# Optimization experiments

Measured on AMD Instinct MI355X. Metric: run time of the kernel, lower is better.

Reference implementation:

```python
import jax, jax.numpy as jnp
import numpy as np

N_NODES = 100000


def _gcn_layer(x, W, b, src, dst, num_nodes):
    """GCNConv: out = D^-1/2 (A+I) D^-1/2 (x @ W) + b.
    src/dst already include self-loops."""
    h = x @ W  # [N, out]
    ones = jnp.ones(src.shape[0], dtype=x.dtype)
    deg = jax.ops.segment_sum(ones, dst, num_segments=num_nodes)  # in-degree incl. self-loop
    dinv = jnp.where(deg > 0, jax.lax.rsqrt(deg), 0.0)
    norm = dinv[src] * dinv[dst]  # [E]
    msg = h[src] * norm[:, None]  # gather + scale, [E, out]
    out = jax.ops.segment_sum(msg, dst, num_segments=num_nodes)  # scatter-add
    return out + b


def setup_inputs() -> dict:
    key = jax.random.key(0)
    k1, k2, k3, k4, k5, k6 = jax.random.split(key, 6)
    in_c, hid_c, out_c = 128, 128, 64  # hidden = 2*out_channels
    n_edges = 1600000
    x = jax.random.normal(k1, (N_NODES, in_c), dtype=jnp.float32)
    edge_index = jax.random.randint(k2, (2, n_edges), 0, N_NODES, dtype=jnp.int64)
    s = 1.0 / np.sqrt(in_c)
    W1 = jax.random.uniform(k3, (in_c, hid_c), jnp.float32, -s, s)
    b1 = jnp.zeros((hid_c,), jnp.float32)
    s2 = 1.0 / np.sqrt(hid_c)
    W2 = jax.random.uniform(k4, (hid_c, out_c), jnp.float32, -s2, s2)
    b2 = jnp.zeros((out_c,), jnp.float32)
    return {"x": x, "edge_index": edge_index, "W1": W1, "b1": b1, "W2": W2, "b2": b2}


def reference(x, edge_index, W1, b1, W2, b2):
    num_nodes = x.shape[0]
    loops = jnp.arange(num_nodes, dtype=edge_index.dtype)
    src = jnp.concatenate([edge_index[0], loops])
    dst = jnp.concatenate([edge_index[1], loops])
    h = jax.nn.relu(_gcn_layer(x, W1, b1, src, dst, num_nodes))
    return _gcn_layer(h, W2, b2, src, dst, num_nodes)
```

## Files before the change

### kernel.cpp

```cpp
#include <hip/hip_runtime.h>
#include <hip/hip_bf16.h>


typedef short bf16x8 __attribute__((ext_vector_type(8)));
typedef float f32x4 __attribute__((ext_vector_type(4)));

__device__ __forceinline__ unsigned pack_bf16_2(float a, float b) {
    unsigned ua = __builtin_bit_cast(unsigned, a);
    unsigned ub = __builtin_bit_cast(unsigned, b);
    ua += 0x7FFFu + ((ua >> 16) & 1u);
    ub += 0x7FFFu + ((ub >> 16) & 1u);
    return (ua >> 16) | (ub & 0xFFFF0000u);
}
__device__ __forceinline__ unsigned short bf16_1(float a) {
    unsigned ua = __builtin_bit_cast(unsigned, a);
    ua += 0x7FFFu + ((ua >> 16) & 1u);
    return (unsigned short)(ua >> 16);
}
__device__ __forceinline__ float bf16_lo(unsigned v) {
    return __builtin_bit_cast(float, v << 16);
}
__device__ __forceinline__ float bf16_hi(unsigned v) {
    return __builtin_bit_cast(float, v & 0xFFFF0000u);
}

__global__ __launch_bounds__(256) void partition_fixed(const int* __restrict__ src,
                                                       const int* __restrict__ dst,
                                                       int* __restrict__ bcur,
                                                       int2* __restrict__ ebuf,
                                                       int E, int nb, int cap) {
    __shared__ int hist[256];
    __shared__ int basel[256];
    const int tid = threadIdx.x;
    const int c0 = blockIdx.x * 4096;
    for (int t = tid; t < nb; t += 256) hist[t] = 0;
    __syncthreads();
    int s[16], d[16], r[16];
#pragma unroll
    for (int i = 0; i < 16; ++i) {
        int idx = c0 + i * 256 + tid;
        if (idx < E) {
            s[i] = src[idx];
            d[i] = dst[idx];
            r[i] = atomicAdd(&hist[d[i] >> 10], 1);
        } else {
            d[i] = -1;
        }
    }
    __syncthreads();
    for (int t = tid; t < nb; t += 256) basel[t] = hist[t] ? atomicAdd(&bcur[t], hist[t]) : 0;
    __syncthreads();
#pragma unroll
    for (int i = 0; i < 16; ++i) {
        if (d[i] >= 0) {
            int b = d[i] >> 10;
            int pos = basel[b] + r[i];
            if (pos < cap)
                ebuf[(size_t)b * cap + pos] = make_int2(s[i], d[i]);
        }
    }
}

__global__ __launch_bounds__(256) void csr_build(const int2* __restrict__ ebuf,
                                                 const int* __restrict__ bcur,
                                                 int* __restrict__ offs,
                                                 float* __restrict__ dinv,
                                                 int* __restrict__ csr,
                                                 int N, int E, int nb, int cap) {
    __shared__ int hist[1024];
    __shared__ int lofs[1024];
    __shared__ int stmp[256];
    __shared__ int s_e0, s_cnt;
    const int b = blockIdx.x;
    const int tid = threadIdx.x;
    const int n0 = b << 10;

    {
        int bc = (tid < nb) ? bcur[tid] : 0;
        stmp[tid] = bc;
        __syncthreads();
        int run = bc;
        for (int off = 1; off < 256; off <<= 1) {
            int t = (tid >= off) ? stmp[tid - off] : 0;
            __syncthreads();
            run += t;
            stmp[tid] = run;
            __syncthreads();
        }
        if (tid == b) { s_cnt = bc; s_e0 = run - bc; }
        __syncthreads();
    }
    const int e0 = s_e0;
    const int cnt = s_cnt;
    const int2* eb = ebuf + (size_t)b * cap;

#pragma unroll
    for (int q = 0; q < 4; ++q) hist[tid + q * 256] = 0;
    __syncthreads();
    for (int e = tid; e < cnt; e += 256)
        atomicAdd(&hist[eb[e].y & 1023], 1);
    __syncthreads();
    const int base4 = tid * 4;
    int v[4];
#pragma unroll
    for (int q = 0; q < 4; ++q) v[q] = hist[base4 + q];
    const int tsum = v[0] + v[1] + v[2] + v[3];
    stmp[tid] = tsum;
    __syncthreads();
    int run = tsum;
    for (int off = 1; off < 256; off <<= 1) {
        int t = (tid >= off) ? stmp[tid - off] : 0;
        __syncthreads();
        run += t;
        stmp[tid] = run;
        __syncthreads();
    }
    int s = run - tsum;
#pragma unroll
    for (int q = 0; q < 4; ++q) { lofs[base4 + q] = s; s += v[q]; }
    __syncthreads();
#pragma unroll
    for (int q = 0; q < 4; ++q) {
        int il = tid + q * 256;
        int node = n0 + il;
        if (node < N) {
            offs[node] = e0 + lofs[il];
            dinv[node] = rsqrtf((float)(hist[il] + 1));
        }
    }
    __syncthreads();
    for (int e = tid; e < cnt; e += 256) {
        int2 p = eb[e];
        int pos = atomicAdd(&lofs[p.y & 1023], 1);
        csr[e0 + pos] = p.x;
    }
    if (b == 0 && tid == 0) offs[N] = E;
}

template <int COUT, bool INBF16>
__global__ __launch_bounds__(256) void gemm_mfma(const void* __restrict__ Xv,
                                                 const float* __restrict__ W,
                                                 const float* __restrict__ dinv,
                                                 unsigned short* __restrict__ Gs, int N) {
    constexpr int BR = 64;
    constexpr int CPT = COUT / 16;
    __shared__ unsigned short sx[BR][136];
    __shared__ unsigned short swT[COUT][136];
    const int tid = threadIdx.x;
    const int r0 = blockIdx.x * BR;

    if constexpr (INBF16) {
        const unsigned* Xb = (const unsigned*)Xv;
#pragma unroll
        for (int q = 0; q < 4; ++q) {
            int off = q * 1024 + tid * 4;
            int row = off >> 6;
            int ku = off & 63;
            size_t grow = (size_t)min(r0 + row, N - 1);
            uint4 v = *reinterpret_cast<const uint4*>(&Xb[grow * 64 + ku]);
            *reinterpret_cast<uint4*>(&sx[row][ku * 2]) = v;
        }
    } else {
        const float* Xf = (const float*)Xv;
#pragma unroll
        for (int q = 0; q < 8; ++q) {
            int off = q * 1024 + tid * 4;
            int row = off >> 7;
            int k = off & 127;
            size_t grow = (size_t)min(r0 + row, N - 1);
            float4 v = *reinterpret_cast<const float4*>(&Xf[grow * 128 + k]);
            uint2 pk;
            pk.x = pack_bf16_2(v.x, v.y);
            pk.y = pack_bf16_2(v.z, v.w);
            *reinterpret_cast<uint2*>(&sx[row][k]) = pk;
        }
    }
#pragma unroll
    for (int q = 0; q < COUT / 8; ++q) {
        int off = q * 1024 + tid * 4;
        int k = off / COUT;
        int c = off % COUT;
        float4 v = *reinterpret_cast<const float4*>(&W[off]);
        swT[c + 0][k] = bf16_1(v.x);
        swT[c + 1][k] = bf16_1(v.y);
        swT[c + 2][k] = bf16_1(v.z);
        swT[c + 3][k] = bf16_1(v.w);
    }
    __syncthreads();

    const int w = tid >> 6;
    const int l = tid & 63;
    const int lr = l & 15;
    const int lkg = l >> 4;
    f32x4 acc[CPT];
#pragma unroll
    for (int c = 0; c < CPT; ++c) acc[c] = f32x4{0.f, 0.f, 0.f, 0.f};

#pragma unroll
    for (int ks = 0; ks < 4; ++ks) {
        const int k0 = ks * 32 + lkg * 8;
        bf16x8 a = *reinterpret_cast<const bf16x8*>(&sx[w * 16 + lr][k0]);
#pragma unroll
        for (int c = 0; c < CPT; ++c) {
            bf16x8 b = *reinterpret_cast<const bf16x8*>(&swT[c * 16 + lr][k0]);
            acc[c] = __builtin_amdgcn_mfma_f32_16x16x32_bf16(a, b, acc[c], 0, 0, 0);
        }
    }

#pragma unroll
    for (int r = 0; r < 4; ++r) {
        int gr = r0 + w * 16 + lkg * 4 + r;
        if (gr < N) {
            float di = dinv[gr];
#pragma unroll
            for (int c = 0; c < CPT; ++c)
                Gs[(size_t)gr * COUT + c * 16 + lr] = bf16_1(acc[c][r] * di);
        }
    }
}

__global__ __launch_bounds__(256) void agg1_kernel(const unsigned* __restrict__ Gb,
                                                   const int* __restrict__ offs,
                                                   const int* __restrict__ csr,
                                                   const float* __restrict__ dinv,
                                                   const float* __restrict__ bias,
                                                   unsigned* __restrict__ outb, int N) {
    int node = (blockIdx.x * blockDim.x + threadIdx.x) >> 6;
    int lane = threadIdx.x & 63;
    if (node >= N) return;
    int e = offs[node];
    const int end = offs[node + 1];
    unsigned sv = Gb[(size_t)node * 64 + lane];
    float ax = bf16_lo(sv), ay = bf16_hi(sv);
    for (; e + 16 <= end; e += 16) {
        int j[16];
#pragma unroll
        for (int q = 0; q < 16; ++q) j[q] = csr[e + q];
        unsigned v[16];
#pragma unroll
        for (int q = 0; q < 16; ++q) v[q] = Gb[(size_t)j[q] * 64 + lane];
#pragma unroll
        for (int q = 0; q < 16; ++q) { ax += bf16_lo(v[q]); ay += bf16_hi(v[q]); }
    }
    for (; e + 8 <= end; e += 8) {
        int j[8];
#pragma unroll
        for (int q = 0; q < 8; ++q) j[q] = csr[e + q];
        unsigned v[8];
#pragma unroll
        for (int q = 0; q < 8; ++q) v[q] = Gb[(size_t)j[q] * 64 + lane];
#pragma unroll
        for (int q = 0; q < 8; ++q) { ax += bf16_lo(v[q]); ay += bf16_hi(v[q]); }
    }
    for (; e + 4 <= end; e += 4) {
        int j0 = csr[e], j1 = csr[e + 1], j2 = csr[e + 2], j3 = csr[e + 3];
        unsigned v0 = Gb[(size_t)j0 * 64 + lane];
        unsigned v1 = Gb[(size_t)j1 * 64 + lane];
        unsigned v2 = Gb[(size_t)j2 * 64 + lane];
        unsigned v3 = Gb[(size_t)j3 * 64 + lane];
        ax += bf16_lo(v0) + bf16_lo(v1) + bf16_lo(v2) + bf16_lo(v3);
        ay += bf16_hi(v0) + bf16_hi(v1) + bf16_hi(v2) + bf16_hi(v3);
    }
    for (; e < end; ++e) {
        unsigned v = Gb[(size_t)csr[e] * 64 + lane];
        ax += bf16_lo(v); ay += bf16_hi(v);
    }
    float di = dinv[node];
    float ox = fmaxf(ax * di + bias[lane * 2 + 0], 0.f);
    float oy = fmaxf(ay * di + bias[lane * 2 + 1], 0.f);
    outb[(size_t)node * 64 + lane] = pack_bf16_2(ox, oy);
}

__global__ __launch_bounds__(256) void agg2_kernel(const unsigned* __restrict__ Gb,
                                                   const int* __restrict__ offs,
                                                   const int* __restrict__ csr,
                                                   const float* __restrict__ dinv,
                                                   const float* __restrict__ bias,
                                                   float* __restrict__ out, int N) {
    int tid = blockIdx.x * blockDim.x + threadIdx.x;
    int node = (tid >> 6) * 2 + ((threadIdx.x >> 5) & 1);
    int c = threadIdx.x & 31;
    if (node >= N) return;
    int e = offs[node];
    const int end = offs[node + 1];
    unsigned sv = Gb[(size_t)node * 32 + c];
    float ax = bf16_lo(sv), ay = bf16_hi(sv);
    for (; e + 16 <= end; e += 16) {
        int j[16];
#pragma unroll
        for (int q = 0; q < 16; ++q) j[q] = csr[e + q];
        unsigned v[16];
#pragma unroll
        for (int q = 0; q < 16; ++q) v[q] = Gb[(size_t)j[q] * 32 + c];
#pragma unroll
        for (int q = 0; q < 16; ++q) { ax += bf16_lo(v[q]); ay += bf16_hi(v[q]); }
    }
    for (; e + 8 <= end; e += 8) {
        int j[8];
#pragma unroll
        for (int q = 0; q < 8; ++q) j[q] = csr[e + q];
        unsigned v[8];
#pragma unroll
        for (int q = 0; q < 8; ++q) v[q] = Gb[(size_t)j[q] * 32 + c];
#pragma unroll
        for (int q = 0; q < 8; ++q) { ax += bf16_lo(v[q]); ay += bf16_hi(v[q]); }
    }
    for (; e + 4 <= end; e += 4) {
        int j0 = csr[e], j1 = csr[e + 1], j2 = csr[e + 2], j3 = csr[e + 3];
        unsigned v0 = Gb[(size_t)j0 * 32 + c];
        unsigned v1 = Gb[(size_t)j1 * 32 + c];
        unsigned v2 = Gb[(size_t)j2 * 32 + c];
        unsigned v3 = Gb[(size_t)j3 * 32 + c];
        ax += bf16_lo(v0) + bf16_lo(v1) + bf16_lo(v2) + bf16_lo(v3);
        ay += bf16_hi(v0) + bf16_hi(v1) + bf16_hi(v2) + bf16_hi(v3);
    }
    for (; e < end; ++e) {
        unsigned v = Gb[(size_t)csr[e] * 32 + c];
        ax += bf16_lo(v); ay += bf16_hi(v);
    }
    float di = dinv[node];
    float2 o;
    o.x = ax * di + bias[c * 2 + 0];
    o.y = ay * di + bias[c * 2 + 1];
    *reinterpret_cast<float2*>(&out[(size_t)node * 64 + c * 2]) = o;
}

extern "C" void kernel_launch(void* const* d_in, const int* in_sizes, int n_in,
                              void* d_out, int out_size, void* d_ws, size_t ws_size,
                              hipStream_t stream) {
    const float* x  = (const float*)d_in[0];
    const int*   ei = (const int*)d_in[1];
    const float* W1 = (const float*)d_in[2];
    const float* b1 = (const float*)d_in[3];
    const float* W2 = (const float*)d_in[4];
    const float* b2 = (const float*)d_in[5];
    float* out = (float*)d_out;

    const int N = in_sizes[0] / 128;
    const int E = in_sizes[1] / 2;
    const int* src = ei;
    const int* dst = ei + E;
    const int nbkt = (N + 1023) >> 10;
    const int cap = E / nbkt + E / (4 * nbkt) + 1024;

    unsigned* g1b = (unsigned*)d_ws;
    unsigned* a1b = g1b + (size_t)N * 64;
    unsigned* g2b = g1b;
    int2* ebuf = (int2*)d_ws;
    char* p = (char*)(a1b + (size_t)N * 64);
    float* dinv = (float*)p; p += (((size_t)N * 4) + 15) & ~(size_t)15;
    int* offs = (int*)p;   p += (((size_t)(N + 1) * 4) + 15) & ~(size_t)15;
    int* csr = (int*)p;    p += (((size_t)E * 4) + 15) & ~(size_t)15;
    int* bcur = (int*)p;   p += (((size_t)256 * 4) + 15) & ~(size_t)15;
    if ((size_t)(p - (char*)d_ws) > ws_size || nbkt > 256 ||
        (size_t)nbkt * cap * 8 > (size_t)N * 64 * 4) return;

    hipMemsetAsync(bcur, 0, 256 * sizeof(int), stream);
    partition_fixed<<<(E + 4095) / 4096, 256, 0, stream>>>(src, dst, bcur, ebuf, E, nbkt, cap);
    csr_build<<<nbkt, 256, 0, stream>>>(ebuf, bcur, offs, dinv, csr, N, E, nbkt, cap);

    gemm_mfma<128, false><<<(N + 63) / 64, 256, 0, stream>>>(
        x, W1, dinv, (unsigned short*)g1b, N);
    agg1_kernel<<<(N + 3) / 4, 256, 0, stream>>>(g1b, offs, csr, dinv, b1, a1b, N);

    gemm_mfma<64, true><<<(N + 63) / 64, 256, 0, stream>>>(
        a1b, W2, dinv, (unsigned short*)g2b, N);
    agg2_kernel<<<(N + 7) / 8, 256, 0, stream>>>(g2b, offs, csr, dinv, b2, out, N);
}
```

Baseline: 220.4 us.

## Fuse bucket partition and CSR build into one cooperative kernel with grid syncs

Replaces the memset plus the two preprocessing kernels (edge partition into buckets, per-bucket CSR build) with one cooperative kernel. The stages are separated by grid-wide syncs, and block 0 zeroes the bucket counters. This is meant to remove two launch/dependency gaps and the separate memset. In exchange it adds grid-sync overhead, needs every block co-resident for the cooperative launch, and leaves the launch's return status unchecked.

```diff
diff --git a/kernel.cpp b/kernel.cpp
--- a/kernel.cpp
+++ b/kernel.cpp
@@ -1,5 +1,8 @@
 #include <hip/hip_runtime.h>
 #include <hip/hip_bf16.h>
+#include <hip/hip_cooperative_groups.h>
+
+namespace cg = cooperative_groups;
 
 
 typedef short bf16x8 __attribute__((ext_vector_type(8)));
@@ -24,62 +27,99 @@
     return __builtin_bit_cast(float, v & 0xFFFF0000u);
 }
 
-__global__ __launch_bounds__(256) void partition_fixed(const int* __restrict__ src,
-                                                       const int* __restrict__ dst,
-                                                       int* __restrict__ bcur,
-                                                       int2* __restrict__ ebuf,
-                                                       int E, int nb, int cap) {
-    __shared__ int hist[256];
-    __shared__ int basel[256];
-    const int tid = threadIdx.x;
-    const int c0 = blockIdx.x * 4096;
-    for (int t = tid; t < nb; t += 256) hist[t] = 0;
-    __syncthreads();
-    int s[16], d[16], r[16];
-#pragma unroll
-    for (int i = 0; i < 16; ++i) {
-        int idx = c0 + i * 256 + tid;
-        if (idx < E) {
-            s[i] = src[idx];
-            d[i] = dst[idx];
-            r[i] = atomicAdd(&hist[d[i] >> 10], 1);
-        } else {
-            d[i] = -1;
-        }
-    }
-    __syncthreads();
-    for (int t = tid; t < nb; t += 256) basel[t] = hist[t] ? atomicAdd(&bcur[t], hist[t]) : 0;
-    __syncthreads();
-#pragma unroll
-    for (int i = 0; i < 16; ++i) {
-        if (d[i] >= 0) {
-            int b = d[i] >> 10;
-            int pos = basel[b] + r[i];
-            if (pos < cap)
-                ebuf[(size_t)b * cap + pos] = make_int2(s[i], d[i]);
-        }
-    }
-}
-
-__global__ __launch_bounds__(256) void csr_build(const int2* __restrict__ ebuf,
-                                                 const int* __restrict__ bcur,
+__global__ __launch_bounds__(256) void prep_coop(const int* __restrict__ src,
+                                                 const int* __restrict__ dst,
+                                                 int* __restrict__ bcur,
+                                                 int2* __restrict__ ebuf,
                                                  int* __restrict__ offs,
                                                  float* __restrict__ dinv,
                                                  int* __restrict__ csr,
                                                  int N, int E, int nb, int cap) {
-    __shared__ int hist[1024];
-    __shared__ int lofs[1024];
-    __shared__ int stmp[256];
-    __shared__ int s_e0, s_cnt;
-    const int b = blockIdx.x;
+    __shared__ int shm[1024 + 1024 + 256 + 2];
+    cg::grid_group grid = cg::this_grid();
     const int tid = threadIdx.x;
-    const int n0 = b << 10;
+
+    if (blockIdx.x == 0) bcur[tid] = 0;
+    grid.sync();
 
     {
-        int bc = (tid < nb) ? bcur[tid] : 0;
-        stmp[tid] = bc;
-        __syncthreads();
-        int run = bc;
+        int* hist = shm;
+        int* basel = shm + 256;
+        for (int c0 = blockIdx.x * 4096; c0 < E; c0 += gridDim.x * 4096) {
+            for (int t = tid; t < nb; t += 256) hist[t] = 0;
+            __syncthreads();
+            int s[16], d[16], r[16];
+#pragma unroll
+            for (int i = 0; i < 16; ++i) {
+                int idx = c0 + i * 256 + tid;
+                if (idx < E) {
+                    s[i] = src[idx];
+                    d[i] = dst[idx];
+                    r[i] = atomicAdd(&hist[d[i] >> 10], 1);
+                } else {
+                    d[i] = -1;
+                }
+            }
+            __syncthreads();
+            for (int t = tid; t < nb; t += 256)
+                basel[t] = hist[t] ? atomicAdd(&bcur[t], hist[t]) : 0;
+            __syncthreads();
+#pragma unroll
+            for (int i = 0; i < 16; ++i) {
+                if (d[i] >= 0) {
+                    int b = d[i] >> 10;
+                    int pos = basel[b] + r[i];
+                    if (pos < cap)
+                        ebuf[(size_t)b * cap + pos] = make_int2(s[i], d[i]);
+                }
+            }
+            __syncthreads();
+        }
+    }
+    grid.sync();
+
+    if (blockIdx.x < (unsigned)nb) {
+        int* hist = shm;
+        int* lofs = shm + 1024;
+        int* stmp = shm + 2048;
+        int* s_e0 = shm + 2304;
+        int* s_cnt = shm + 2305;
+        const int b = blockIdx.x;
+        const int n0 = b << 10;
+
+        {
+            int bc = (tid < nb) ? bcur[tid] : 0;
+            stmp[tid] = bc;
+            __syncthreads();
+            int run = bc;
+            for (int off = 1; off < 256; off <<= 1) {
+                int t = (tid >= off) ? stmp[tid - off] : 0;
+                __syncthreads();
+                run += t;
+                stmp[tid] = run;
+                __syncthreads();
+            }
+            if (tid == b) { *s_cnt = bc; *s_e0 = run - bc; }
+            __syncthreads();
+        }
+        const int e0 = *s_e0;
+        const int cnt = *s_cnt;
+        const int2* eb = ebuf + (size_t)b * cap;
+
+#pragma unroll
+        for (int q = 0; q < 4; ++q) hist[tid + q * 256] = 0;
+        __syncthreads();
+        for (int e = tid; e < cnt; e += 256)
+            atomicAdd(&hist[eb[e].y & 1023], 1);
+        __syncthreads();
+        const int base4 = tid * 4;
+        int v[4];
+#pragma unroll
+        for (int q = 0; q < 4; ++q) v[q] = hist[base4 + q];
+        const int tsum = v[0] + v[1] + v[2] + v[3];
+        stmp[tid] = tsum;
+        __syncthreads();
+        int run = tsum;
         for (int off = 1; off < 256; off <<= 1) {
             int t = (tid >= off) ? stmp[tid - off] : 0;
             __syncthreads();
@@ -87,54 +127,27 @@
             stmp[tid] = run;
             __syncthreads();
         }
-        if (tid == b) { s_cnt = bc; s_e0 = run - bc; }
-        __syncthreads();
-    }
-    const int e0 = s_e0;
-    const int cnt = s_cnt;
-    const int2* eb = ebuf + (size_t)b * cap;
-
-#pragma unroll
-    for (int q = 0; q < 4; ++q) hist[tid + q * 256] = 0;
-    __syncthreads();
-    for (int e = tid; e < cnt; e += 256)
-        atomicAdd(&hist[eb[e].y & 1023], 1);
-    __syncthreads();
-    const int base4 = tid * 4;
-    int v[4];
-#pragma unroll
-    for (int q = 0; q < 4; ++q) v[q] = hist[base4 + q];
-    const int tsum = v[0] + v[1] + v[2] + v[3];
-    stmp[tid] = tsum;
-    __syncthreads();
-    int run = tsum;
-    for (int off = 1; off < 256; off <<= 1) {
-        int t = (tid >= off) ? stmp[tid - off] : 0;
-        __syncthreads();
-        run += t;
-        stmp[tid] = run;
-        __syncthreads();
-    }
-    int s = run - tsum;
-#pragma unroll
-    for (int q = 0; q < 4; ++q) { lofs[base4 + q] = s; s += v[q]; }
-    __syncthreads();
-#pragma unroll
-    for (int q = 0; q < 4; ++q) {
-        int il = tid + q * 256;
-        int node = n0 + il;
-        if (node < N) {
-            offs[node] = e0 + lofs[il];
-            dinv[node] = rsqrtf((float)(hist[il] + 1));
-        }
-    }
-    __syncthreads();
-    for (int e = tid; e < cnt; e += 256) {
-        int2 p = eb[e];
-        int pos = atomicAdd(&lofs[p.y & 1023], 1);
-        csr[e0 + pos] = p.x;
-    }
-    if (b == 0 && tid == 0) offs[N] = E;
+        int s = run - tsum;
+#pragma unroll
+        for (int q = 0; q < 4; ++q) { lofs[base4 + q] = s; s += v[q]; }
+        __syncthreads();
+#pragma unroll
+        for (int q = 0; q < 4; ++q) {
+            int il = tid + q * 256;
+            int node = n0 + il;
+            if (node < N) {
+                offs[node] = e0 + lofs[il];
+                dinv[node] = rsqrtf((float)(hist[il] + 1));
+            }
+        }
+        __syncthreads();
+        for (int e = tid; e < cnt; e += 256) {
+            int2 p = eb[e];
+            int pos = atomicAdd(&lofs[p.y & 1023], 1);
+            csr[e0 + pos] = p.x;
+        }
+        if (b == 0 && tid == 0) offs[N] = E;
+    }
 }
 
 template <int COUT, bool INBF16>
@@ -355,9 +368,16 @@
     if ((size_t)(p - (char*)d_ws) > ws_size || nbkt > 256 ||
         (size_t)nbkt * cap * 8 > (size_t)N * 64 * 4) return;
 
-    hipMemsetAsync(bcur, 0, 256 * sizeof(int), stream);
-    partition_fixed<<<(E + 4095) / 4096, 256, 0, stream>>>(src, dst, bcur, ebuf, E, nbkt, cap);
-    csr_build<<<nbkt, 256, 0, stream>>>(ebuf, bcur, offs, dinv, csr, N, E, nbkt, cap);
+    {
+        int nchunk = (E + 4095) / 4096;
+        int nblk = nchunk > nbkt ? nchunk : nbkt;
+        int N_ = N, E_ = E, nb_ = nbkt, cap_ = cap;
+        void* args[] = {(void*)&src, (void*)&dst, (void*)&bcur, (void*)&ebuf,
+                        (void*)&offs, (void*)&dinv, (void*)&csr,
+                        (void*)&N_, (void*)&E_, (void*)&nb_, (void*)&cap_};
+        hipLaunchCooperativeKernel((void*)prep_coop, dim3(nblk), dim3(256),
+                                   args, 0, stream);
+    }
 
     gemm_mfma<128, false><<<(N + 63) / 64, 256, 0, stream>>>(
         x, W1, dinv, (unsigned short*)g1b, N);
```

After: 310.9 us. 1.41x slower.

## Replace global-atomic bucket partition with per-chunk fixed slots for CSR build

Applied to the files above, without the earlier changes.

The partition kernel now writes each 4096-edge chunk's edges into fixed per-(bucket,chunk) slots of capacity CHUNK_CAP and records per-chunk counts, instead of reserving space with global atomics on a bucket cursor. The CSR build kernel sums the per-chunk counts to get bucket offsets and walks the chunk slots serially per thread. This drops the memset and the global atomics and makes ordering deterministic, but edges beyond CHUNK_CAP per chunk-bucket are silently dropped. The serial per-chunk loops in csr_build also give low parallelism: each thread walks about 40 edges in sequence.

```diff
diff --git a/kernel.cpp b/kernel.cpp
--- a/kernel.cpp
+++ b/kernel.cpp
@@ -4,6 +4,8 @@
 
 typedef short bf16x8 __attribute__((ext_vector_type(8)));
 typedef float f32x4 __attribute__((ext_vector_type(4)));
+
+#define CHUNK_CAP 112
 
 __device__ __forceinline__ unsigned pack_bf16_2(float a, float b) {
     unsigned ua = __builtin_bit_cast(unsigned, a);
@@ -24,15 +26,15 @@
     return __builtin_bit_cast(float, v & 0xFFFF0000u);
 }
 
-__global__ __launch_bounds__(256) void partition_fixed(const int* __restrict__ src,
-                                                       const int* __restrict__ dst,
-                                                       int* __restrict__ bcur,
-                                                       int2* __restrict__ ebuf,
-                                                       int E, int nb, int cap) {
+__global__ __launch_bounds__(256) void partition_det(const int* __restrict__ src,
+                                                     const int* __restrict__ dst,
+                                                     int* __restrict__ pcnt,
+                                                     int2* __restrict__ ebuf,
+                                                     int E, int nb, int nchunk) {
     __shared__ int hist[256];
-    __shared__ int basel[256];
     const int tid = threadIdx.x;
-    const int c0 = blockIdx.x * 4096;
+    const int c = blockIdx.x;
+    const int c0 = c * 4096;
     for (int t = tid; t < nb; t += 256) hist[t] = 0;
     __syncthreads();
     int s[16], d[16], r[16];
@@ -48,66 +50,41 @@
         }
     }
     __syncthreads();
-    for (int t = tid; t < nb; t += 256) basel[t] = hist[t] ? atomicAdd(&bcur[t], hist[t]) : 0;
-    __syncthreads();
+    for (int t = tid; t < nb; t += 256)
+        pcnt[(size_t)t * nchunk + c] = min(hist[t], CHUNK_CAP);
 #pragma unroll
     for (int i = 0; i < 16; ++i) {
-        if (d[i] >= 0) {
+        if (d[i] >= 0 && r[i] < CHUNK_CAP) {
             int b = d[i] >> 10;
-            int pos = basel[b] + r[i];
-            if (pos < cap)
-                ebuf[(size_t)b * cap + pos] = make_int2(s[i], d[i]);
-        }
-    }
-}
-
-__global__ __launch_bounds__(256) void csr_build(const int2* __restrict__ ebuf,
-                                                 const int* __restrict__ bcur,
-                                                 int* __restrict__ offs,
-                                                 float* __restrict__ dinv,
-                                                 int* __restrict__ csr,
-                                                 int N, int E, int nb, int cap) {
+            ebuf[((size_t)b * nchunk + c) * CHUNK_CAP + r[i]] = make_int2(s[i], d[i]);
+        }
+    }
+}
+
+__global__ __launch_bounds__(256) void csr_build_det(const int2* __restrict__ ebuf,
+                                                     const int* __restrict__ pcnt,
+                                                     int* __restrict__ offs,
+                                                     float* __restrict__ dinv,
+                                                     int* __restrict__ csr,
+                                                     int N, int E, int nb, int nchunk) {
     __shared__ int hist[1024];
     __shared__ int lofs[1024];
+    __shared__ int scnt[1024];
     __shared__ int stmp[256];
-    __shared__ int s_e0, s_cnt;
+    __shared__ int s_e0;
     const int b = blockIdx.x;
     const int tid = threadIdx.x;
     const int n0 = b << 10;
 
-    {
-        int bc = (tid < nb) ? bcur[tid] : 0;
-        stmp[tid] = bc;
-        __syncthreads();
-        int run = bc;
-        for (int off = 1; off < 256; off <<= 1) {
-            int t = (tid >= off) ? stmp[tid - off] : 0;
-            __syncthreads();
-            run += t;
-            stmp[tid] = run;
-            __syncthreads();
-        }
-        if (tid == b) { s_cnt = bc; s_e0 = run - bc; }
-        __syncthreads();
-    }
-    const int e0 = s_e0;
-    const int cnt = s_cnt;
-    const int2* eb = ebuf + (size_t)b * cap;
-
-#pragma unroll
-    for (int q = 0; q < 4; ++q) hist[tid + q * 256] = 0;
-    __syncthreads();
-    for (int e = tid; e < cnt; e += 256)
-        atomicAdd(&hist[eb[e].y & 1023], 1);
-    __syncthreads();
-    const int base4 = tid * 4;
-    int v[4];
-#pragma unroll
-    for (int q = 0; q < 4; ++q) v[q] = hist[base4 + q];
-    const int tsum = v[0] + v[1] + v[2] + v[3];
-    stmp[tid] = tsum;
-    __syncthreads();
-    int run = tsum;
+    for (int c = tid; c < nchunk; c += 256) scnt[c] = pcnt[(size_t)b * nchunk + c];
+    int tot = 0;
+    if (tid < nb) {
+        const int* row = pcnt + (size_t)tid * nchunk;
+        for (int c = 0; c < nchunk; ++c) tot += row[c];
+    }
+    stmp[tid] = tot;
+    __syncthreads();
+    int run = tot;
     for (int off = 1; off < 256; off <<= 1) {
         int t = (tid >= off) ? stmp[tid - off] : 0;
         __syncthreads();
@@ -115,6 +92,35 @@
         stmp[tid] = run;
         __syncthreads();
     }
+    if (tid == b) s_e0 = run - tot;
+    __syncthreads();
+    const int e0 = s_e0;
+
+#pragma unroll
+    for (int q = 0; q < 4; ++q) hist[tid + q * 256] = 0;
+    __syncthreads();
+    for (int c = tid; c < nchunk; c += 256) {
+        const int2* eb = ebuf + ((size_t)b * nchunk + c) * CHUNK_CAP;
+        const int m = scnt[c];
+        for (int s2 = 0; s2 < m; ++s2)
+            atomicAdd(&hist[eb[s2].y & 1023], 1);
+    }
+    __syncthreads();
+    const int base4 = tid * 4;
+    int v[4];
+#pragma unroll
+    for (int q = 0; q < 4; ++q) v[q] = hist[base4 + q];
+    const int tsum = v[0] + v[1] + v[2] + v[3];
+    stmp[tid] = tsum;
+    __syncthreads();
+    run = tsum;
+    for (int off = 1; off < 256; off <<= 1) {
+        int t = (tid >= off) ? stmp[tid - off] : 0;
+        __syncthreads();
+        run += t;
+        stmp[tid] = run;
+        __syncthreads();
+    }
     int s = run - tsum;
 #pragma unroll
     for (int q = 0; q < 4; ++q) { lofs[base4 + q] = s; s += v[q]; }
@@ -129,10 +135,14 @@
         }
     }
     __syncthreads();
-    for (int e = tid; e < cnt; e += 256) {
-        int2 p = eb[e];
-        int pos = atomicAdd(&lofs[p.y & 1023], 1);
-        csr[e0 + pos] = p.x;
+    for (int c = tid; c < nchunk; c += 256) {
+        const int2* eb = ebuf + ((size_t)b * nchunk + c) * CHUNK_CAP;
+        const int m = scnt[c];
+        for (int s2 = 0; s2 < m; ++s2) {
+            int2 p = eb[s2];
+            int pos = atomicAdd(&lofs[p.y & 1023], 1);
+            csr[e0 + pos] = p.x;
+        }
     }
     if (b == 0 && tid == 0) offs[N] = E;
 }
@@ -341,7 +351,7 @@
     const int* src = ei;
     const int* dst = ei + E;
     const int nbkt = (N + 1023) >> 10;
-    const int cap = E / nbkt + E / (4 * nbkt) + 1024;
+    const int nchunk = (E + 4095) / 4096;
 
     unsigned* g1b = (unsigned*)d_ws;
     unsigned* a1b = g1b + (size_t)N * 64;
@@ -351,13 +361,12 @@
     float* dinv = (float*)p; p += (((size_t)N * 4) + 15) & ~(size_t)15;
     int* offs = (int*)p;   p += (((size_t)(N + 1) * 4) + 15) & ~(size_t)15;
     int* csr = (int*)p;    p += (((size_t)E * 4) + 15) & ~(size_t)15;
-    int* bcur = (int*)p;   p += (((size_t)256 * 4) + 15) & ~(size_t)15;
-    if ((size_t)(p - (char*)d_ws) > ws_size || nbkt > 256 ||
-        (size_t)nbkt * cap * 8 > (size_t)N * 64 * 4) return;
-
-    hipMemsetAsync(bcur, 0, 256 * sizeof(int), stream);
-    partition_fixed<<<(E + 4095) / 4096, 256, 0, stream>>>(src, dst, bcur, ebuf, E, nbkt, cap);
-    csr_build<<<nbkt, 256, 0, stream>>>(ebuf, bcur, offs, dinv, csr, N, E, nbkt, cap);
+    int* pcnt = (int*)p;   p += (((size_t)nbkt * nchunk * 4) + 15) & ~(size_t)15;
+    if ((size_t)(p - (char*)d_ws) > ws_size || nbkt > 256 || nchunk > 1024 ||
+        (size_t)nbkt * nchunk * CHUNK_CAP * 8 > (size_t)N * 64 * 4 * 2) return;
+
+    partition_det<<<nchunk, 256, 0, stream>>>(src, dst, pcnt, ebuf, E, nbkt, nchunk);
+    csr_build_det<<<nbkt, 256, 0, stream>>>(ebuf, pcnt, offs, dinv, csr, N, E, nbkt, nchunk);
 
     gemm_mfma<128, false><<<(N + 63) / 64, 256, 0, stream>>>(
         x, W1, dinv, (unsigned short*)g1b, N);
```

Result: slower. 256.4 us (+16.3%).
